# Performance work log

Hardware: AMD Instinct MI355X
Metric: run time of the kernel (lower is better)

Reference implementation:

```python
import jax, jax.numpy as jnp
import numpy as np

B, T, DIM, HEADS, DH = 4, 2048, 1024, 16, 64  # dh = dim // heads


def setup_inputs() -> dict:
    key = jax.random.key(0)
    k1, k2, k3 = jax.random.split(key, 3)
    x = jax.random.normal(k1, (B, T, DIM), dtype=jnp.float32)
    # nn.Linear weights, stored as [in, out] for x @ W convention
    W_qkv = jax.random.normal(k2, (DIM, 3 * HEADS * DH), dtype=jnp.float32) * (DIM ** -0.5)
    W_o = jax.random.normal(k3, (HEADS * DH, DIM), dtype=jnp.float32) * ((HEADS * DH) ** -0.5)
    return {"x": x, "W_qkv": W_qkv, "W_o": W_o}


def reference(x, W_qkv, W_o):
    b, t, _ = x.shape
    qkv = x @ W_qkv  # [b, t, 3*h*dh]
    # einops 'b t (d k h) -> k b h t d' with k=3, h=HEADS: fused axis splits as (dh, 3, h)
    qkv = qkv.reshape(b, t, DH, 3, HEADS)
    qkv = jnp.transpose(qkv, (3, 0, 4, 1, 2))  # [3, b, h, t, dh]
    q, k, v = qkv[0], qkv[1], qkv[2]
    scale = DH ** -0.5
    scores = jnp.einsum('bhid,bhjd->bhij', q, k) * scale  # [b, h, t, t]
    attn = jax.nn.softmax(scores, axis=-1)
    out = jnp.einsum('bhij,bhjd->bhid', attn, v)  # [b, h, t, dh]
    out = jnp.transpose(out, (0, 2, 1, 3)).reshape(b, t, HEADS * DH)  # 'b h t d -> b t (h d)'
    return out @ W_o
```

## Files before the change

kernel.cpp:

```cpp
#include <hip/hip_runtime.h>

typedef __bf16 bf16;
typedef __bf16 bf16x2 __attribute__((ext_vector_type(2)));
typedef __bf16 bf16x4 __attribute__((ext_vector_type(4)));
typedef __bf16 bf16x8 __attribute__((ext_vector_type(8)));
typedef float  f32x4  __attribute__((ext_vector_type(4)));
typedef float  f32x16 __attribute__((ext_vector_type(16)));
typedef unsigned int u32;
typedef unsigned int u32x2 __attribute__((ext_vector_type(2)));
typedef unsigned int u32x4 __attribute__((ext_vector_type(4)));

#define LOG2E 1.44269504088896340736f
#define EXP_SC (0.125f * LOG2E)

#if __has_builtin(__builtin_amdgcn_exp2f)
#define EXP2F(x) __builtin_amdgcn_exp2f(x)
#else
#define EXP2F(x) __builtin_exp2f(x)
#endif

__device__ __forceinline__ u32 pk_bf16(float lo, float hi) {
  u32 a = __float_as_uint(lo) + 0x8000u;
  u32 b = __float_as_uint(hi) + 0x8000u;
  return __builtin_amdgcn_perm(b, a, 0x07060302);
}
#if __has_builtin(__builtin_amdgcn_cvt_pk_bf16_f32)
__device__ __forceinline__ u32 cvtpk(float lo, float hi) {
  bf16x2 t = __builtin_amdgcn_cvt_pk_bf16_f32(lo, hi);
  return __builtin_bit_cast(u32, t);
}
#else
__device__ __forceinline__ u32 cvtpk(float lo, float hi) { return pk_bf16(lo, hi); }
#endif
__device__ __forceinline__ unsigned short bf16r(float x) {
  return (unsigned short)((__float_as_uint(x) + 0x8000u) >> 16);
}

__device__ __forceinline__ f32x16 zero16() {
  f32x16 a;
#pragma unroll
  for (int i = 0; i < 16; i++) a[i] = 0.f;
  return a;
}

__device__ __forceinline__ void async_ld16(void* lds, const void* g) {
  __builtin_amdgcn_global_load_lds(
      (const __attribute__((address_space(1))) void*)(g),
      (__attribute__((address_space(3))) void*)(lds),
      16, 0, 0);
}

__global__ void prep_all(const float* __restrict__ x,    bf16* __restrict__ xb,
                         const float* __restrict__ Wqkv, bf16* __restrict__ wqkvT,
                         const float* __restrict__ Wo,   bf16* __restrict__ woT) {
  __shared__ float s[12288];
  const int bid = blockIdx.x;
  const int tid = threadIdx.x;
  if (bid < 8192) {
    int i = bid * 256 + tid;
    float4 v = ((const float4*)x)[i];
    u32x2 o = { pk_bf16(v.x, v.y), pk_bf16(v.z, v.w) };
    *(u32x2*)(xb + (size_t)i * 4) = o;
  } else if (bid < 8448) {
    const int k0 = (bid - 8192) * 4;
    for (int i = tid; i < 3072; i += 256) {
      int r = i / 768, c = (i - r * 768) * 4;
      *(float4*)(s + r * 3072 + c) = *(const float4*)(Wqkv + (size_t)(k0 + r) * 3072 + c);
    }
    __syncthreads();
    for (int n = tid; n < 3072; n += 256) {
      int d = n & 63, h = (n >> 6) & 15, wch = n >> 10;
      int on = d * 48 + wch * 16 + h;
      u32x2 v = { pk_bf16(s[0 * 3072 + on], s[1 * 3072 + on]),
                  pk_bf16(s[2 * 3072 + on], s[3 * 3072 + on]) };
      *(u32x2*)(wqkvT + (size_t)n * 1024 + k0) = v;
    }
  } else {
    const int k0 = (bid - 8448) * 8;
    for (int i = tid; i < 2048; i += 256) {
      int r = i >> 8, c = (i & 255) * 4;
      *(float4*)(s + r * 1024 + c) = *(const float4*)(Wo + (size_t)(k0 + r) * 1024 + c);
    }
    __syncthreads();
    for (int n = tid; n < 1024; n += 256) {
      u32x4 v = { pk_bf16(s[0 * 1024 + n], s[1 * 1024 + n]),
                  pk_bf16(s[2 * 1024 + n], s[3 * 1024 + n]),
                  pk_bf16(s[4 * 1024 + n], s[5 * 1024 + n]),
                  pk_bf16(s[6 * 1024 + n], s[7 * 1024 + n]) };
      *(u32x4*)(woT + (size_t)n * 1024 + k0) = v;
    }
  }
}

template <int MODE>
__launch_bounds__(256, 2)
__global__ void gemm_bt(const bf16* __restrict__ A, const bf16* __restrict__ BT,
                        float* __restrict__ C, int N,
                        bf16* __restrict__ Qb, bf16* __restrict__ Kb, bf16* __restrict__ Vb) {
  constexpr int K = 1024;
  __shared__ bf16 sA[128 * 64];
  __shared__ bf16 sB[128 * 64];
  const int m0 = blockIdx.x * 128;
  const int n0 = blockIdx.y * 128;
  const int tid = threadIdx.x;
  const int lane = tid & 63;
  const int w = tid >> 6;
  const int wm = (w >> 1) * 64, wn = (w & 1) * 64;
  const int l15 = lane & 15, quad = lane >> 4;

  f32x4 acc[4][4];
  for (int i = 0; i < 4; i++)
    for (int j = 0; j < 4; j++) acc[i][j] = f32x4{0.f, 0.f, 0.f, 0.f};

  const int rT = tid >> 3;
  const int jT = (tid & 7) ^ (rT & 7);
  const bf16* gA = A  + (size_t)(m0 + rT) * K + jT * 8;
  const bf16* gB = BT + (size_t)(n0 + rT) * K + jT * 8;

  for (int k0 = 0; k0 < K; k0 += 64) {
    __syncthreads();
    for (int i = 0; i < 4; i++) {
      async_ld16((void*)(sA + (i * 256 + w * 64) * 8), gA + (size_t)i * 32 * K);
      async_ld16((void*)(sB + (i * 256 + w * 64) * 8), gB + (size_t)i * 32 * K);
    }
    gA += 64; gB += 64;
    __syncthreads();

    for (int kk = 0; kk < 2; kk++) {
      bf16x8 af[4], bfr[4];
      for (int ms = 0; ms < 4; ms++) {
        int r = wm + ms * 16 + l15;
        af[ms] = *(const bf16x8*)(sA + r * 64 + (((kk * 4 + quad) ^ (r & 7)) * 8));
      }
      for (int ns = 0; ns < 4; ns++) {
        int r = wn + ns * 16 + l15;
        bfr[ns] = *(const bf16x8*)(sB + r * 64 + (((kk * 4 + quad) ^ (r & 7)) * 8));
      }
      for (int ms = 0; ms < 4; ms++)
        for (int ns = 0; ns < 4; ns++)
          acc[ms][ns] = __builtin_amdgcn_mfma_f32_16x16x32_bf16(af[ms], bfr[ns], acc[ms][ns], 0, 0, 0);
    }
  }

  if (MODE == 0) {
    for (int ms = 0; ms < 4; ms++)
      for (int ns = 0; ns < 4; ns++)
        for (int r = 0; r < 4; r++) {
          int row = m0 + wm + ms * 16 + quad * 4 + r;
          int col = n0 + wn + ns * 16 + l15;
          C[(size_t)row * N + col] = acc[ms][ns][r];
        }
  } else {
    for (int ms = 0; ms < 4; ms++)
      for (int ns = 0; ns < 4; ns++)
        for (int r = 0; r < 4; r++) {
          int row = m0 + wm + ms * 16 + quad * 4 + r;
          int col = n0 + wn + ns * 16 + l15;
          int b = row >> 11, t = row & 2047;
          int d = col & 63, h = (col >> 6) & 15, wch = col >> 10;
          bf16* dst = (wch == 0) ? Qb : (wch == 1) ? Kb : Vb;
          float v = acc[ms][ns][r] * ((wch == 0) ? EXP_SC : 1.0f);
          size_t idx = (wch == 2)
              ? ((((size_t)(b * 16 + h)) * 64 + d) * 2048 + t)
              : ((((size_t)(b * 16 + h)) * 2048 + t) * 64 + d);
          ((unsigned short*)dst)[idx] = bf16r(v);
        }
  }
}

__launch_bounds__(256, 3)
__global__ void attn_fwd(const bf16* __restrict__ Q, const bf16* __restrict__ K,
                         const bf16* __restrict__ VT, bf16* __restrict__ O) {
  __shared__ bf16 sK[64 * 64];
  __shared__ bf16 sV[4][64 * 64];
  const int bh = blockIdx.x;
  const int q0 = blockIdx.y * 128;
  const int tid = threadIdx.x;
  const int lane = tid & 63, w = tid >> 6;
  const int l31 = lane & 31, hi = lane >> 5;

  bf16x8 qf[4];
  {
    const bf16* qp = Q + ((size_t)bh * 2048 + q0 + w * 32 + l31) * 64 + hi * 8;
#pragma unroll
    for (int kq = 0; kq < 4; kq++) qf[kq] = *(const bf16x8*)(qp + kq * 16);
  }

  f32x16 oacc[2];
  oacc[0] = zero16(); oacc[1] = zero16();
  float rs = 0.f;

  const int cA = w * 128 + lane;
  const int rA = cA >> 3, jA = (cA & 7) ^ (rA & 7);
  const bf16* gK = K  + ((size_t)bh * 2048 + rA) * 64 + jA * 8;
  const bf16* gV = VT + ((size_t)bh * 64 + rA) * 2048 + jA * 8;

  int fo[2][4];
#pragma unroll
  for (int sub = 0; sub < 2; sub++)
#pragma unroll
    for (int st = 0; st < 4; st++) {
      int r = sub * 32 + l31;
      fo[sub][st] = r * 64 + (((st * 2 + hi) ^ (r & 7)) * 8);
    }

  async_ld16((void*)(sK + w * 1024),           gK);
  async_ld16((void*)(sK + w * 1024 + 512),     gK + 512);
  async_ld16((void*)(sV[0] + w * 1024),        gV);
  async_ld16((void*)(sV[0] + w * 1024 + 512),  gV + 16384);
  gK += 4096; gV += 64;

  for (int t = 0; t < 32; t++) {
    __syncthreads();
    bf16x8 kf[2][4];
#pragma unroll
    for (int ks = 0; ks < 2; ks++)
#pragma unroll
      for (int kq = 0; kq < 4; kq++)
        kf[ks][kq] = *(const bf16x8*)(sK + fo[ks][kq]);
    __syncthreads();
    const bf16* vb = sV[t & 3];
    if (t < 31) {
      bf16* vn = (bf16*)sV[(t + 1) & 3];
      async_ld16((void*)(sK + w * 1024),          gK);
      async_ld16((void*)(sK + w * 1024 + 512),    gK + 512);
      async_ld16((void*)(vn + w * 1024),          gV);
      async_ld16((void*)(vn + w * 1024 + 512),    gV + 16384);
      gK += 4096; gV += 64;
    }

    f32x16 S[2];
#pragma unroll
    for (int ks = 0; ks < 2; ks++) {
      f32x16 a = zero16();
      a = __builtin_amdgcn_mfma_f32_32x32x16_bf16(kf[ks][0], qf[0], a, 0, 0, 0);
      a = __builtin_amdgcn_mfma_f32_32x32x16_bf16(kf[ks][1], qf[1], a, 0, 0, 0);
      a = __builtin_amdgcn_mfma_f32_32x32x16_bf16(kf[ks][2], qf[2], a, 0, 0, 0);
      a = __builtin_amdgcn_mfma_f32_32x32x16_bf16(kf[ks][3], qf[3], a, 0, 0, 0);
      S[ks] = a;
    }

    bf16x8 vf[2][4];
#pragma unroll
    for (int ds = 0; ds < 2; ds++)
#pragma unroll
      for (int kk = 0; kk < 4; kk++)
        vf[ds][kk] = *(const bf16x8*)(vb + fo[ds][kk]);

    bf16x8 F[4];
#pragma unroll
    for (int ks = 0; ks < 2; ks++) {
      float p[16];
#pragma unroll
      for (int r = 0; r < 16; r++) p[r] = EXP2F(S[ks][r]);
      rs += (((p[0] + p[1]) + (p[2] + p[3])) + ((p[4] + p[5]) + (p[6] + p[7])))
          + (((p[8] + p[9]) + (p[10] + p[11])) + ((p[12] + p[13]) + (p[14] + p[15])));
      u32 c0 = cvtpk(p[0],  p[1]),  c1 = cvtpk(p[2],  p[3]);
      u32 c2 = cvtpk(p[4],  p[5]),  c3 = cvtpk(p[6],  p[7]);
      u32 c4 = cvtpk(p[8],  p[9]),  c5 = cvtpk(p[10], p[11]);
      u32 c6 = cvtpk(p[12], p[13]), c7 = cvtpk(p[14], p[15]);
      asm("v_permlane32_swap_b32 %0, %1" : "+v"(c0), "+v"(c2));
      asm("v_permlane32_swap_b32 %0, %1" : "+v"(c1), "+v"(c3));
      asm("v_permlane32_swap_b32 %0, %1" : "+v"(c4), "+v"(c6));
      asm("v_permlane32_swap_b32 %0, %1" : "+v"(c5), "+v"(c7));
      u32x4 f0 = { c0, c1, c2, c3 };
      u32x4 f1 = { c4, c5, c6, c7 };
      F[ks * 2 + 0] = __builtin_bit_cast(bf16x8, f0);
      F[ks * 2 + 1] = __builtin_bit_cast(bf16x8, f1);
    }

#pragma unroll
    for (int ds = 0; ds < 2; ds++) {
      f32x16 a = oacc[ds];
      a = __builtin_amdgcn_mfma_f32_32x32x16_bf16(vf[ds][0], F[0], a, 0, 0, 0);
      a = __builtin_amdgcn_mfma_f32_32x32x16_bf16(vf[ds][1], F[1], a, 0, 0, 0);
      a = __builtin_amdgcn_mfma_f32_32x32x16_bf16(vf[ds][2], F[2], a, 0, 0, 0);
      a = __builtin_amdgcn_mfma_f32_32x32x16_bf16(vf[ds][3], F[3], a, 0, 0, 0);
      oacc[ds] = a;
    }
  }

  float rt = rs + __shfl_xor(rs, 32, 64);
  float inv = 1.0f / rt;
  const int b = bh >> 4, h = bh & 15;
  const int trow = q0 + w * 32 + l31;
#pragma unroll
  for (int ds = 0; ds < 2; ds++)
#pragma unroll
    for (int g = 0; g < 4; g++) {
      int d = ds * 32 + g * 8 + hi * 4;
      u32x2 pkv = { cvtpk(oacc[ds][g * 4 + 0] * inv, oacc[ds][g * 4 + 1] * inv),
                    cvtpk(oacc[ds][g * 4 + 2] * inv, oacc[ds][g * 4 + 3] * inv) };
      *(u32x2*)(O + ((size_t)b * 2048 + trow) * 1024 + h * 64 + d) = pkv;
    }
}

extern "C" void kernel_launch(void* const* d_in, const int* in_sizes, int n_in,
                              void* d_out, int out_size, void* d_ws, size_t ws_size,
                              hipStream_t stream) {
  const float* x    = (const float*)d_in[0];
  const float* Wqkv = (const float*)d_in[1];
  const float* Wo   = (const float*)d_in[2];
  float* out = (float*)d_out;
  char* ws = (char*)d_ws;

  bf16* wqkvT = (bf16*)(ws);
  bf16* woT   = (bf16*)(ws + 6291456);
  bf16* xb    = (bf16*)(ws + 8388608);
  bf16* Qb    = (bf16*)(ws + 25165824);
  bf16* Kb    = (bf16*)(ws + 41943040);
  bf16* VTb   = (bf16*)(ws + 58720256);
  bf16* AOb   = xb;

  prep_all<<<8576, 256, 0, stream>>>(x, xb, Wqkv, wqkvT, Wo, woT);
  gemm_bt<1><<<dim3(64, 24), 256, 0, stream>>>(xb, wqkvT, nullptr, 3072, Qb, Kb, VTb);
  attn_fwd<<<dim3(64, 16), 256, 0, stream>>>(Qb, Kb, VTb, AOb);
  gemm_bt<0><<<dim3(64, 8), 256, 0, stream>>>(AOb, woT, out, 1024, nullptr, nullptr, nullptr);
}
```

Measured before the change: 281.5 us.

## Software-pipeline QK^T and PV across tiles; vectorize QKV epilogue stores

The attention loop is restructured so each iteration computes the QK^T scores of the current key tile while applying exp and the PV MFMA to the previous tile, with s_setprio raised around the MFMA blocks. The aim is to overlap exp/VALU work with matrix-core work. Separately, the QKV weight columns are permuted within each head's d dimension so the GEMM epilogue can write four contiguous bf16 values per store to Q/K and to transposed V, replacing scalar scattered stores. The ping-pong score buffers add register pressure, and the explicit prologue and epilogue add code size.

```diff
diff --git a/kernel.cpp b/kernel.cpp
--- a/kernel.cpp
+++ b/kernel.cpp
@@ -69,7 +69,8 @@
     }
     __syncthreads();
     for (int n = tid; n < 3072; n += 256) {
-      int d = n & 63, h = (n >> 6) & 15, wch = n >> 10;
+      int dl = n & 63, h = (n >> 6) & 15, wch = n >> 10;
+      int d = ((dl & 15) << 2) | (dl >> 4);
       int on = d * 48 + wch * 16 + h;
       u32x2 v = { pk_bf16(s[0 * 3072 + on], s[1 * 3072 + on]),
                   pk_bf16(s[2 * 3072 + on], s[3 * 3072 + on]) };
@@ -151,20 +152,33 @@
           C[(size_t)row * N + col] = acc[ms][ns][r];
         }
   } else {
-    for (int ms = 0; ms < 4; ms++)
-      for (int ns = 0; ns < 4; ns++)
+    const int col0 = n0 + wn;
+    const int wch = col0 >> 10;
+    const int h = (col0 >> 6) & 15;
+    if (wch != 2) {
+      bf16* dst = (wch == 0) ? Qb : Kb;
+      const float sc = (wch == 0) ? EXP_SC : 1.0f;
+      for (int ms = 0; ms < 4; ms++)
         for (int r = 0; r < 4; r++) {
           int row = m0 + wm + ms * 16 + quad * 4 + r;
-          int col = n0 + wn + ns * 16 + l15;
           int b = row >> 11, t = row & 2047;
-          int d = col & 63, h = (col >> 6) & 15, wch = col >> 10;
-          bf16* dst = (wch == 0) ? Qb : (wch == 1) ? Kb : Vb;
-          float v = acc[ms][ns][r] * ((wch == 0) ? EXP_SC : 1.0f);
-          size_t idx = (wch == 2)
-              ? ((((size_t)(b * 16 + h)) * 64 + d) * 2048 + t)
-              : ((((size_t)(b * 16 + h)) * 2048 + t) * 64 + d);
-          ((unsigned short*)dst)[idx] = bf16r(v);
+          u32x2 v = { cvtpk(acc[ms][0][r] * sc, acc[ms][1][r] * sc),
+                      cvtpk(acc[ms][2][r] * sc, acc[ms][3][r] * sc) };
+          *(u32x2*)((unsigned short*)dst +
+                    (((size_t)(b * 16 + h)) * 2048 + t) * 64 + l15 * 4) = v;
         }
+    } else {
+      for (int ms = 0; ms < 4; ms++)
+        for (int ns = 0; ns < 4; ns++) {
+          int row = m0 + wm + ms * 16 + quad * 4;
+          int b = row >> 11, t = row & 2047;
+          int d = l15 * 4 + ns;
+          u32x2 v = { cvtpk(acc[ms][ns][0], acc[ms][ns][1]),
+                      cvtpk(acc[ms][ns][2], acc[ms][ns][3]) };
+          *(u32x2*)((unsigned short*)Vb +
+                    (((size_t)(b * 16 + h)) * 64 + d) * 2048 + t) = v;
+        }
+    }
   }
 }
 
@@ -210,44 +224,7 @@
   async_ld16((void*)(sV[0] + w * 1024 + 512),  gV + 16384);
   gK += 4096; gV += 64;
 
-  for (int t = 0; t < 32; t++) {
-    __syncthreads();
-    bf16x8 kf[2][4];
-#pragma unroll
-    for (int ks = 0; ks < 2; ks++)
-#pragma unroll
-      for (int kq = 0; kq < 4; kq++)
-        kf[ks][kq] = *(const bf16x8*)(sK + fo[ks][kq]);
-    __syncthreads();
-    const bf16* vb = sV[t & 3];
-    if (t < 31) {
-      bf16* vn = (bf16*)sV[(t + 1) & 3];
-      async_ld16((void*)(sK + w * 1024),          gK);
-      async_ld16((void*)(sK + w * 1024 + 512),    gK + 512);
-      async_ld16((void*)(vn + w * 1024),          gV);
-      async_ld16((void*)(vn + w * 1024 + 512),    gV + 16384);
-      gK += 4096; gV += 64;
-    }
-
-    f32x16 S[2];
-#pragma unroll
-    for (int ks = 0; ks < 2; ks++) {
-      f32x16 a = zero16();
-      a = __builtin_amdgcn_mfma_f32_32x32x16_bf16(kf[ks][0], qf[0], a, 0, 0, 0);
-      a = __builtin_amdgcn_mfma_f32_32x32x16_bf16(kf[ks][1], qf[1], a, 0, 0, 0);
-      a = __builtin_amdgcn_mfma_f32_32x32x16_bf16(kf[ks][2], qf[2], a, 0, 0, 0);
-      a = __builtin_amdgcn_mfma_f32_32x32x16_bf16(kf[ks][3], qf[3], a, 0, 0, 0);
-      S[ks] = a;
-    }
-
-    bf16x8 vf[2][4];
-#pragma unroll
-    for (int ds = 0; ds < 2; ds++)
-#pragma unroll
-      for (int kk = 0; kk < 4; kk++)
-        vf[ds][kk] = *(const bf16x8*)(vb + fo[ds][kk]);
-
-    bf16x8 F[4];
+  auto expF = [&](f32x16 (&S)[2], bf16x8 (&F)[4]) {
 #pragma unroll
     for (int ks = 0; ks < 2; ks++) {
       float p[16];
@@ -268,7 +245,106 @@
       F[ks * 2 + 0] = __builtin_bit_cast(bf16x8, f0);
       F[ks * 2 + 1] = __builtin_bit_cast(bf16x8, f1);
     }
-
+  };
+
+  auto step = [&](int t, f32x16 (&Scur)[2], f32x16 (&Sprev)[2]) {
+    __syncthreads();
+    bf16x8 kf[2][4];
+#pragma unroll
+    for (int ks = 0; ks < 2; ks++)
+#pragma unroll
+      for (int kq = 0; kq < 4; kq++)
+        kf[ks][kq] = *(const bf16x8*)(sK + fo[ks][kq]);
+    __syncthreads();
+    if (t < 31) {
+      bf16* vn = (bf16*)sV[(t + 1) & 3];
+      async_ld16((void*)(sK + w * 1024),          gK);
+      async_ld16((void*)(sK + w * 1024 + 512),    gK + 512);
+      async_ld16((void*)(vn + w * 1024),          gV);
+      async_ld16((void*)(vn + w * 1024 + 512),    gV + 16384);
+      gK += 4096; gV += 64;
+    }
+    __builtin_amdgcn_s_setprio(1);
+#pragma unroll
+    for (int ks = 0; ks < 2; ks++) {
+      f32x16 a = zero16();
+      a = __builtin_amdgcn_mfma_f32_32x32x16_bf16(kf[ks][0], qf[0], a, 0, 0, 0);
+      a = __builtin_amdgcn_mfma_f32_32x32x16_bf16(kf[ks][1], qf[1], a, 0, 0, 0);
+      a = __builtin_amdgcn_mfma_f32_32x32x16_bf16(kf[ks][2], qf[2], a, 0, 0, 0);
+      a = __builtin_amdgcn_mfma_f32_32x32x16_bf16(kf[ks][3], qf[3], a, 0, 0, 0);
+      Scur[ks] = a;
+    }
+    __builtin_amdgcn_s_setprio(0);
+    const bf16* vb = sV[(t - 1) & 3];
+    bf16x8 vf[2][4];
+#pragma unroll
+    for (int ds = 0; ds < 2; ds++)
+#pragma unroll
+      for (int kk = 0; kk < 4; kk++)
+        vf[ds][kk] = *(const bf16x8*)(vb + fo[ds][kk]);
+    bf16x8 F[4];
+    expF(Sprev, F);
+    __builtin_amdgcn_s_setprio(1);
+#pragma unroll
+    for (int ds = 0; ds < 2; ds++) {
+      f32x16 a = oacc[ds];
+      a = __builtin_amdgcn_mfma_f32_32x32x16_bf16(vf[ds][0], F[0], a, 0, 0, 0);
+      a = __builtin_amdgcn_mfma_f32_32x32x16_bf16(vf[ds][1], F[1], a, 0, 0, 0);
+      a = __builtin_amdgcn_mfma_f32_32x32x16_bf16(vf[ds][2], F[2], a, 0, 0, 0);
+      a = __builtin_amdgcn_mfma_f32_32x32x16_bf16(vf[ds][3], F[3], a, 0, 0, 0);
+      oacc[ds] = a;
+    }
+    __builtin_amdgcn_s_setprio(0);
+  };
+
+  f32x16 SA[2], SB[2];
+
+  {
+    __syncthreads();
+    bf16x8 kf[2][4];
+#pragma unroll
+    for (int ks = 0; ks < 2; ks++)
+#pragma unroll
+      for (int kq = 0; kq < 4; kq++)
+        kf[ks][kq] = *(const bf16x8*)(sK + fo[ks][kq]);
+    __syncthreads();
+    {
+      bf16* vn = (bf16*)sV[1];
+      async_ld16((void*)(sK + w * 1024),          gK);
+      async_ld16((void*)(sK + w * 1024 + 512),    gK + 512);
+      async_ld16((void*)(vn + w * 1024),          gV);
+      async_ld16((void*)(vn + w * 1024 + 512),    gV + 16384);
+      gK += 4096; gV += 64;
+    }
+    __builtin_amdgcn_s_setprio(1);
+#pragma unroll
+    for (int ks = 0; ks < 2; ks++) {
+      f32x16 a = zero16();
+      a = __builtin_amdgcn_mfma_f32_32x32x16_bf16(kf[ks][0], qf[0], a, 0, 0, 0);
+      a = __builtin_amdgcn_mfma_f32_32x32x16_bf16(kf[ks][1], qf[1], a, 0, 0, 0);
+      a = __builtin_amdgcn_mfma_f32_32x32x16_bf16(kf[ks][2], qf[2], a, 0, 0, 0);
+      a = __builtin_amdgcn_mfma_f32_32x32x16_bf16(kf[ks][3], qf[3], a, 0, 0, 0);
+      SA[ks] = a;
+    }
+    __builtin_amdgcn_s_setprio(0);
+  }
+
+  for (int t = 1; t < 31; t += 2) {
+    step(t,     SB, SA);
+    step(t + 1, SA, SB);
+  }
+  step(31, SB, SA);
+
+  {
+    const bf16* vb = sV[31 & 3];
+    bf16x8 vf[2][4];
+#pragma unroll
+    for (int ds = 0; ds < 2; ds++)
+#pragma unroll
+      for (int kk = 0; kk < 4; kk++)
+        vf[ds][kk] = *(const bf16x8*)(vb + fo[ds][kk]);
+    bf16x8 F[4];
+    expF(SB, F);
 #pragma unroll
     for (int ds = 0; ds < 2; ds++) {
       f32x16 a = oacc[ds];
```

Result: slower. 313.6 us (+11.4%).
